# Kernel optimization log

Measured on AMD Instinct MI355X. Metric: run time of the kernel, lower is better.

## Reference

```python
import jax, jax.numpy as jnp
import numpy as np

WEIGHT_DECAY = 1e-4


def setup_inputs() -> dict:
    key = jax.random.key(0)
    k1, k2, k3 = jax.random.split(key, 3)
    # Linear weights: [out_features, in_features]
    w1 = jax.random.normal(k1, (4096, 4096), dtype=jnp.float32)
    w2 = jax.random.normal(k2, (8192, 2048), dtype=jnp.float32)
    w3 = jax.random.normal(k3, (2048, 8192), dtype=jnp.float32)
    return {"w1": w1, "w2": w2, "w3": w3}


def _spectral_norm(w):
    # torch.svd(weight) -> s sorted descending; max(s) == top singular value.
    s = jnp.linalg.svd(w, compute_uv=False)
    return jnp.max(s)


def reference(w1, w2, w3):
    # sum of largest singular values over all Linear weights, scaled by weight_decay
    spectral_reg = _spectral_norm(w1) + _spectral_norm(w2) + _spectral_norm(w3)
    return WEIGHT_DECAY * spectral_reg
```

## Files before the change

kernel.cpp:

```cpp
#include <hip/hip_runtime.h>
#include <math.h>


#define K_STEPS 24
#define VCAP 8192
#define MELEMS 16777216

#define UOFF   0
#define V0OFF  (3 * VCAP)
#define WOFF   (6 * VCAP)
#define P8OFF  (9 * VCAP)
#define P8TOT  3670016
#define BASOFF (P8OFF + P8TOT)
#define AL8OFF (BASOFF + 3 * K_STEPS * VCAP)
#define B28OFF (AL8OFF + 3 * K_STEPS)
#define NS2OFF (B28OFF + 3 * (K_STEPS + 1))
#define RQ2OFF (NS2OFF + 3)
#define VEC8_FLOATS (RQ2OFF + 3)

#define FB_AOFF (12 * VCAP)

typedef unsigned int u32;
typedef unsigned short u16;
typedef float f32x2 __attribute__((ext_vector_type(2)));

__device__ __forceinline__ int matN(int m) { return m == 0 ? 4096 : (m == 1 ? 2048 : 8192); }
__device__ __forceinline__ int pbase(int m) { return m == 0 ? 0 : (m == 1 ? 1048576 : 1572864); }

__device__ __forceinline__ f32x2 up8(u32 w, bool hi) {
    return hi ? __builtin_amdgcn_cvt_pk_f32_fp8(w, true)
              : __builtin_amdgcn_cvt_pk_f32_fp8(w, false);
}

__device__ float blockReduce(float v) {
    __shared__ float sh[16];
    int lane = threadIdx.x & 63, wid = threadIdx.x >> 6;
#pragma unroll
    for (int off = 32; off; off >>= 1) v += __shfl_down(v, off, 64);
    if (lane == 0) sh[wid] = v;
    __syncthreads();
    if (wid == 0) {
        int nw = (blockDim.x + 63) >> 6;
        float x = (lane < nw) ? sh[lane] : 0.0f;
#pragma unroll
        for (int off = 8; off; off >>= 1) x += __shfl_down(x, off, 64);
        if (lane == 0) sh[0] = x;
    }
    __syncthreads();
    float r = sh[0];
    __syncthreads();
    return r;
}


__global__ __launch_bounds__(1024) void k_init8(float* vec) {
    int bid = blockIdx.x, tid = threadIdx.x;
    if (bid < 3) {
        int mat = bid, n = matN(mat);
        float acc = 0.0f;
        for (int i = tid; i < VCAP; i += 1024) {
            float val = 0.0f;
            if (i < n) {
                unsigned h = (unsigned)(i * 2654435761u) ^ (0x9E3779B9u * (unsigned)(mat + 1));
                h ^= h >> 16; h *= 0x85EBCA6Bu; h ^= h >> 13; h *= 0xC2B2AE35u; h ^= h >> 16;
                val = ((h >> 8) * (1.0f / 16777216.0f)) - 0.5f;
                acc += val * val;
            }
            vec[UOFF + mat * VCAP + i] = val;
            vec[V0OFF + mat * VCAP + i] = 0.0f;
        }
        float nrm2 = blockReduce(acc);
        if (tid == 0) vec[B28OFF + mat * (K_STEPS + 1)] = nrm2;
    } else {
        for (int i = tid; i < 3 * K_STEPS; i += 1024) vec[AL8OFF + i] = 0.0f;
        for (int i = tid; i < 3 * (K_STEPS + 1); i += 1024)
            if (i % (K_STEPS + 1)) vec[B28OFF + i] = 0.0f;
        if (tid < 3) { vec[NS2OFF + tid] = 0.0f; vec[RQ2OFF + tid] = 0.0f; }
    }
}

__global__ __launch_bounds__(256) void k_convert8(const float* __restrict__ A0,
                                                  const float* __restrict__ A1,
                                                  const float* __restrict__ A2,
                                                  u32* __restrict__ F) {
    const int per_mat = MELEMS >> 3;
    const int nvec = 3 * per_mat;
    for (int i = blockIdx.x * 256 + threadIdx.x; i < nvec; i += gridDim.x * 256) {
        int mat = i >> 21;
        int iv = i & (per_mat - 1);
        const float4* Af = (const float4*)(mat == 0 ? A0 : (mat == 1 ? A1 : A2));
        float4 a = Af[2 * iv], b = Af[2 * iv + 1];
        u32 lo = __builtin_amdgcn_cvt_pk_fp8_f32(a.x, a.y, 0u, false);
        lo = __builtin_amdgcn_cvt_pk_fp8_f32(a.z, a.w, lo, true);
        u32 hi = __builtin_amdgcn_cvt_pk_fp8_f32(b.x, b.y, 0u, false);
        hi = __builtin_amdgcn_cvt_pk_fp8_f32(b.z, b.w, hi, true);
        uint2 o; o.x = lo; o.y = hi;
        ((uint2*)F)[i] = o;
    }
}

template <int N, int R>
__device__ void fusedAT_body(const u32* __restrict__ Fm, float* __restrict__ vec,
                             int mat, int chunk, int j,
                             float* __restrict__ Pm, float* wsh, float* shA) {
    constexpr int RPW = R / 4;
    constexpr int NU4 = N >> 4;
    constexpr int KK  = N >> 11;
    const int tid = threadIdx.x, wv = tid >> 6, lane = tid & 63;
    const int row0 = chunk * R;

    float inv = rsqrtf(vec[B28OFF + mat * (K_STEPS + 1) + j]);
    const float4* vp = (const float4*)(vec + UOFF + mat * VCAP);
    float aacc = 0.0f;
#pragma unroll
    for (int rr = 0; rr < RPW; ++rr) {
        int rl = wv * RPW + rr;
        const uint4* rp = (const uint4*)((const char*)Fm + (size_t)(row0 + rl) * N);
        float s = 0.0f;
#pragma unroll
        for (int c = lane; c < NU4; c += 64) {
            uint4 a = rp[c];
            float4 u0 = vp[4 * c + 0], u1 = vp[4 * c + 1];
            float4 u2 = vp[4 * c + 2], u3 = vp[4 * c + 3];
            f32x2 f0 = up8(a.x, false), f1 = up8(a.x, true);
            f32x2 f2 = up8(a.y, false), f3 = up8(a.y, true);
            f32x2 f4 = up8(a.z, false), f5 = up8(a.z, true);
            f32x2 f6 = up8(a.w, false), f7 = up8(a.w, true);
            s += f0[0] * u0.x + f0[1] * u0.y + f1[0] * u0.z + f1[1] * u0.w
               + f2[0] * u1.x + f2[1] * u1.y + f3[0] * u1.z + f3[1] * u1.w
               + f4[0] * u2.x + f4[1] * u2.y + f5[0] * u2.z + f5[1] * u2.w
               + f6[0] * u3.x + f6[1] * u3.y + f7[0] * u3.z + f7[1] * u3.w;
        }
#pragma unroll
        for (int off = 32; off; off >>= 1) s += __shfl_down(s, off, 64);
        if (lane == 0) { wsh[rl] = s * inv; aacc += s * s; }
    }
    if (lane == 0) shA[wv] = aacc;
    __syncthreads();
    if (tid == 0)
        atomicAdd(&vec[AL8OFF + mat * K_STEPS + j],
                  (shA[0] + shA[1] + shA[2] + shA[3]) * inv * inv);

#pragma unroll
    for (int kk = 0; kk < KK; ++kk) {
        int col = (tid + (kk << 8)) << 3;
        const char* bb = (const char*)Fm + (size_t)row0 * N + col;
        float a0 = 0, a1 = 0, a2 = 0, a3 = 0, a4 = 0, a5 = 0, a6 = 0, a7 = 0;
#pragma unroll 8
        for (int r = 0; r < R; ++r) {
            uint2 a = *(const uint2*)(bb + (size_t)r * N);
            f32x2 f0 = up8(a.x, false), f1 = up8(a.x, true);
            f32x2 f2 = up8(a.y, false), f3 = up8(a.y, true);
            float w = wsh[r];
            a0 += f0[0] * w; a1 += f0[1] * w; a2 += f1[0] * w; a3 += f1[1] * w;
            a4 += f2[0] * w; a5 += f2[1] * w; a6 += f3[0] * w; a7 += f3[1] * w;
        }
        float* Pp = Pm + (size_t)chunk * N + col;
        float4 lo = {a0, a1, a2, a3}, hi = {a4, a5, a6, a7};
        ((float4*)Pp)[0] = lo;
        ((float4*)Pp)[1] = hi;
    }
}

__global__ __launch_bounds__(256) void k_fusedAT(const u32* __restrict__ F,
                                                 float* __restrict__ vec, int j) {
    __shared__ float wsh[32];
    __shared__ float shA[4];
    int bid = blockIdx.x;
    if (bid < 256) {
        fusedAT_body<4096, 16>((const u32*)((const char*)F + (size_t)0 * MELEMS),
                               vec, 0, bid, j, vec + P8OFF + pbase(0), wsh, shA);
    } else if (bid < 512) {
        fusedAT_body<2048, 32>((const u32*)((const char*)F + (size_t)1 * MELEMS),
                               vec, 1, bid - 256, j, vec + P8OFF + pbase(1), wsh, shA);
    } else {
        fusedAT_body<8192, 8>((const u32*)((const char*)F + (size_t)2 * MELEMS),
                              vec, 2, bid - 512, j, vec + P8OFF + pbase(2), wsh, shA);
    }
}

__global__ __launch_bounds__(256) void k_stepR8(float* __restrict__ vec, int j) {
    int bid = blockIdx.x, tid = threadIdx.x;
    int mat, col0, n;
    if (bid < 16)      { mat = 0; n = 4096; col0 = bid << 8; }
    else if (bid < 24) { mat = 1; n = 2048; col0 = (bid - 16) << 8; }
    else               { mat = 2; n = 8192; col0 = (bid - 24) << 8; }
    int col = col0 + tid;
    const float* P = vec + P8OFF + pbase(mat);
    float z = 0.0f;
#pragma unroll 8
    for (int rc = 0; rc < 256; ++rc) z += P[(size_t)rc * n + col];
    float b2p = vec[B28OFF + mat * (K_STEPS + 1) + j];
    float bp = sqrtf(b2p);
    float inv = 1.0f / bp;
    float alpha = vec[AL8OFF + mat * K_STEPS + j];
    int g = mat * VCAP + col;
    float v1 = vec[UOFF + g] * inv;
    float r = z - alpha * v1 - bp * vec[V0OFF + g];
    vec[V0OFF + g] = v1;
    vec[UOFF + g] = r;
    vec[BASOFF + (mat * K_STEPS + j) * VCAP + col] = v1;
    float rr2 = blockReduce(r * r);
    if (tid == 0) atomicAdd(&vec[B28OFF + mat * (K_STEPS + 1) + j + 1], rr2);
}

__global__ __launch_bounds__(256) void k_final3(float* __restrict__ vec) {
    int bid = blockIdx.x;
    int mat = bid >> 2, q = bid & 3, tid = threadIdx.x, lane = tid & 63, wv = tid >> 6;
    int n = matN(mat);
    __shared__ double sa[K_STEPS], sb[K_STEPS];
    __shared__ double lamS;
    __shared__ float yl[K_STEPS];
    if (tid < K_STEPS) {
        sa[tid] = (double)vec[AL8OFF + mat * K_STEPS + tid];
        sb[tid] = (tid < K_STEPS - 1)
            ? sqrt((double)vec[B28OFF + mat * (K_STEPS + 1) + tid + 1]) : 0.0;
    }
    __syncthreads();
    if (wv == 0) {
        double g = 0.0;
        if (lane < K_STEPS) {
            double bl = lane ? sb[lane - 1] : 0.0;
            g = sa[lane] + bl + sb[lane];
        }
#pragma unroll
        for (int off = 32; off; off >>= 1) {
            double o = __shfl_xor(g, off, 64);
            if (o > g) g = o;
        }
        double lo = 0.0, hi = g > 0.0 ? g : 1.0;
        for (int round = 0; round < 4; ++round) {
            double step = (hi - lo) / 65.0;
            double x = lo + step * (double)(lane + 1);
            int cnt = 0;
            double d = 1.0;
            for (int i = 0; i < K_STEPS; ++i) {
                double off2 = 0.0;
                if (i) { double b = sb[i - 1]; off2 = b * b / d; }
                d = (sa[i] - x) - off2;
                if (d == 0.0) d = -1e-300;
                if (d < 0.0) cnt++;
            }
            unsigned long long mask = __ballot(cnt >= K_STEPS);
            if (mask) {
                int idx = __ffsll(mask) - 1;
                hi = lo + step * (double)(idx + 1);
                lo = lo + step * (double)idx;
            } else {
                lo = lo + step * 64.0;
            }
        }
        if (lane == 0) lamS = 0.5 * (lo + hi);
    }
    __syncthreads();
    if (tid == 0) {
        double lam2 = lamS * (1.0 + 1e-7);
        double x[K_STEPS], cp[K_STEPS];
        for (int i = 0; i < K_STEPS; ++i) x[i] = 1.0;
        for (int it = 0; it < 3; ++it) {
            double d = sa[0] - lam2;
            if (fabs(d) < 1e-14) d = (d < 0.0 ? -1e-14 : 1e-14);
            cp[0] = sb[0] / d;
            x[0] = x[0] / d;
            for (int i = 1; i < K_STEPS; ++i) {
                double m = (sa[i] - lam2) - sb[i - 1] * cp[i - 1];
                if (fabs(m) < 1e-14) m = (m < 0.0 ? -1e-14 : 1e-14);
                if (i < K_STEPS - 1) cp[i] = sb[i] / m;
                x[i] = (x[i] - sb[i - 1] * x[i - 1]) / m;
            }
            for (int i = K_STEPS - 2; i >= 0; --i) x[i] -= cp[i] * x[i + 1];
            double nr = 0.0;
            for (int i = 0; i < K_STEPS; ++i) nr += x[i] * x[i];
            nr = 1.0 / sqrt(nr);
            for (int i = 0; i < K_STEPS; ++i) x[i] *= nr;
        }
        for (int i = 0; i < K_STEPS; ++i) yl[i] = (float)x[i];
    }
    __syncthreads();
    int qn = n >> 2;
    int c0 = q * qn, c1 = c0 + qn;
    const float* BAS = vec + BASOFF + mat * K_STEPS * VCAP;
    float ns = 0.0f;
    for (int c = c0 + tid; c < c1; c += 256) {
        float acc = 0.0f;
#pragma unroll
        for (int jj = 0; jj < K_STEPS; ++jj) acc += yl[jj] * BAS[jj * VCAP + c];
        vec[WOFF + mat * VCAP + c] = acc;
        ns += acc * acc;
    }
    float t = blockReduce(ns);
    if (tid == 0) atomicAdd(&vec[NS2OFF + mat], t);
}

__global__ __launch_bounds__(1024) void k_rq(const float* __restrict__ A0,
                                             const float* __restrict__ A1,
                                             const float* __restrict__ A2,
                                             float* __restrict__ vec) {
    __shared__ float shA[16];
    int bid = blockIdx.x, tid = threadIdx.x, wv = tid >> 6, lane = tid & 63;
    int mat, row0, n;
    if (bid < 256)      { mat = 0; n = 4096; row0 = bid << 4; }
    else if (bid < 768) { mat = 1; n = 2048; row0 = (bid - 256) << 4; }
    else                { mat = 2; n = 8192; row0 = (bid - 768) << 4; }
    const float* A = mat == 0 ? A0 : (mat == 1 ? A1 : A2);
    int row = row0 + wv;
    const float4* rp = (const float4*)(A + (size_t)row * n);
    const float4* vp = (const float4*)(vec + WOFF + mat * VCAP);
    int nf4 = n >> 2;
    float s = 0.0f;
    for (int c = lane; c < nf4; c += 64) {
        float4 a = rp[c], v = vp[c];
        s += a.x * v.x + a.y * v.y + a.z * v.z + a.w * v.w;
    }
#pragma unroll
    for (int off = 32; off; off >>= 1) s += __shfl_down(s, off, 64);
    if (lane == 0) shA[wv] = s * s;
    __syncthreads();
    if (tid == 0) {
        float t = 0.0f;
#pragma unroll
        for (int k = 0; k < 16; ++k) t += shA[k];
        atomicAdd(&vec[RQ2OFF + mat], t);
    }
}

__global__ void k_out(const float* __restrict__ vec, float* __restrict__ out) {
    if (threadIdx.x == 0 && blockIdx.x == 0) {
        float s = 0.0f;
        for (int m = 0; m < 3; ++m)
            s += sqrtf(vec[RQ2OFF + m] / vec[NS2OFF + m]);
        out[0] = 1e-4f * s;
    }
}

__global__ __launch_bounds__(1024) void k_init(float* vec) {
    int mat = blockIdx.x;
    int n = matN(mat);
    float* V0 = vec + mat * VCAP;
    float* V1 = vec + 3 * VCAP + mat * VCAP;
    float* Z  = vec + 9 * VCAP + mat * VCAP;
    int tid = threadIdx.x;
    float acc = 0.0f;
    for (int i = tid; i < VCAP; i += 1024) {
        float val = 0.0f;
        if (i < n) {
            unsigned h = (unsigned)(i * 2654435761u) ^ (0x9E3779B9u * (unsigned)(mat + 1));
            h ^= h >> 16; h *= 0x85EBCA6Bu; h ^= h >> 13; h *= 0xC2B2AE35u; h ^= h >> 16;
            val = ((h >> 8) * (1.0f / 16777216.0f)) - 0.5f;
            acc += val * val;
        }
        V1[i] = val; V0[i] = 0.0f; Z[i] = 0.0f;
    }
    float nrm2 = blockReduce(acc);
    float inv = rsqrtf(nrm2);
    for (int i = tid; i < n; i += 1024) V1[i] *= inv;
}

__global__ __launch_bounds__(256) void k_gemvA(const float* __restrict__ A0,
                                               const float* __restrict__ A1,
                                               const float* __restrict__ A2,
                                               float* __restrict__ vec) {
    const float* V1 = vec + 3 * VCAP;
    float* W = vec + 6 * VCAP;
    int wid = (int)((blockIdx.x * blockDim.x + threadIdx.x) >> 6);
    int lane = threadIdx.x & 63;
    int mat, row;
    if (wid < 4096)       { mat = 0; row = wid; }
    else if (wid < 12288) { mat = 1; row = wid - 4096; }
    else                  { mat = 2; row = wid - 12288; }
    const float* A = mat == 0 ? A0 : (mat == 1 ? A1 : A2);
    int n = matN(mat);
    const float4* rowp = (const float4*)(A + (size_t)row * n);
    const float4* vp = (const float4*)(V1 + mat * VCAP);
    int nf4 = n >> 2;
    float s = 0.0f;
    for (int t = lane; t < nf4; t += 64) {
        float4 a = rowp[t], v = vp[t];
        s += a.x * v.x + a.y * v.y + a.z * v.z + a.w * v.w;
    }
#pragma unroll
    for (int off = 32; off; off >>= 1) s += __shfl_down(s, off, 64);
    if (lane == 0) W[mat * VCAP + row] = s;
}

__global__ __launch_bounds__(256) void k_gemvT(const float* __restrict__ A0,
                                               const float* __restrict__ A1,
                                               const float* __restrict__ A2,
                                               float* __restrict__ vec) {
    const float* W = vec + 6 * VCAP;
    float* Z = vec + 9 * VCAP;
    int bid = blockIdx.x;
    int mat = bid >> 8;
    int t = bid & 255;
    int n = matN(mat);
    int nColTiles = n >> 10;
    int colTile = t % nColTiles;
    int rowChunk = t / nColTiles;
    int r0 = rowChunk * 64;
    int col = colTile * 1024 + threadIdx.x * 4;
    const float* A = mat == 0 ? A0 : (mat == 1 ? A1 : A2);
    __shared__ float wsh[64];
    if (threadIdx.x < 64) wsh[threadIdx.x] = W[mat * VCAP + r0 + threadIdx.x];
    __syncthreads();
    const float* Ab = A + (size_t)r0 * n + col;
    float4 s = {0.0f, 0.0f, 0.0f, 0.0f};
#pragma unroll 4
    for (int r = 0; r < 64; ++r) {
        float4 a = *(const float4*)(Ab + (size_t)r * n);
        float w = wsh[r];
        s.x += a.x * w; s.y += a.y * w; s.z += a.z * w; s.w += a.w * w;
    }
    float* Zm = Z + mat * VCAP + col;
    atomicAdd(Zm + 0, s.x);
    atomicAdd(Zm + 1, s.y);
    atomicAdd(Zm + 2, s.z);
    atomicAdd(Zm + 3, s.w);
}

__global__ __launch_bounds__(1024) void k_update(float* __restrict__ vec, int j) {
    int mat = blockIdx.x;
    int n = matN(mat);
    float* V0 = vec + mat * VCAP;
    float* V1 = vec + 3 * VCAP + mat * VCAP;
    float* Z  = vec + 9 * VCAP + mat * VCAP;
    float* ALPHA = vec + FB_AOFF;
    float* BETA  = ALPHA + 3 * K_STEPS;
    int tid = threadIdx.x;
    float acc = 0.0f;
    for (int i = tid; i < n; i += 1024) acc += V1[i] * Z[i];
    float alpha = blockReduce(acc);
    float bp = (j > 0) ? BETA[mat * K_STEPS + j - 1] : 0.0f;
    float acc2 = 0.0f;
    for (int i = tid; i < n; i += 1024) {
        float v1 = V1[i];
        float r = Z[i] - alpha * v1 - bp * V0[i];
        V0[i] = v1;
        Z[i] = r;
        acc2 += r * r;
    }
    float b2 = blockReduce(acc2);
    float beta = sqrtf(b2);
    float inv = (beta > 1e-20f) ? (1.0f / beta) : 0.0f;
    for (int i = tid; i < n; i += 1024) {
        V1[i] = Z[i] * inv;
        Z[i] = 0.0f;
    }
    if (tid == 0) {
        ALPHA[mat * K_STEPS + j] = alpha;
        BETA[mat * K_STEPS + j] = beta;
    }
}

__global__ __launch_bounds__(256) void k_final2(const float* __restrict__ vec,
                                                float* __restrict__ out) {
    __shared__ double sa[3][K_STEPS], sb[3][K_STEPS];
    __shared__ double sig[3];
    int tid = threadIdx.x, wid = tid >> 6, lane = tid & 63;
    if (wid < 3 && lane < K_STEPS) {
        const float* AL = vec + FB_AOFF + wid * K_STEPS;
        const float* BE = vec + FB_AOFF + 3 * K_STEPS + wid * K_STEPS;
        sa[wid][lane] = (double)AL[lane];
        sb[wid][lane] = (lane < K_STEPS - 1) ? (double)BE[lane] : 0.0;
    }
    __syncthreads();
    if (wid < 3) {
        double g = 0.0;
        if (lane < K_STEPS) {
            double bl_ = lane ? sb[wid][lane - 1] : 0.0;
            g = sa[wid][lane] + bl_ + sb[wid][lane];
        }
#pragma unroll
        for (int off = 32; off; off >>= 1) {
            double o = __shfl_xor(g, off, 64);
            if (o > g) g = o;
        }
        double lo = 0.0, hi = g > 0.0 ? g : 1.0;
        for (int round = 0; round < 4; ++round) {
            double step = (hi - lo) / 65.0;
            double x = lo + step * (double)(lane + 1);
            int cnt = 0;
            double d = 1.0;
            for (int i = 0; i < K_STEPS; ++i) {
                double off2 = 0.0;
                if (i) { double b = sb[wid][i - 1]; off2 = b * b / d; }
                d = (sa[wid][i] - x) - off2;
                if (d == 0.0) d = -1e-300;
                if (d < 0.0) cnt++;
            }
            unsigned long long mask = __ballot(cnt >= K_STEPS);
            if (mask) {
                int idx = __ffsll(mask) - 1;
                hi = lo + step * (double)(idx + 1);
                lo = lo + step * (double)idx;
            } else {
                lo = lo + step * 64.0;
            }
        }
        if (lane == 0) {
            double lam = 0.5 * (lo + hi);
            sig[wid] = sqrt(lam > 0.0 ? lam : 0.0);
        }
    }
    __syncthreads();
    if (tid == 0) out[0] = (float)(1e-4 * (sig[0] + sig[1] + sig[2]));
}

extern "C" void kernel_launch(void* const* d_in, const int* in_sizes, int n_in,
                              void* d_out, int out_size, void* d_ws, size_t ws_size,
                              hipStream_t stream) {
    const float* A0 = (const float*)d_in[0];
    const float* A1 = (const float*)d_in[1];
    const float* A2 = (const float*)d_in[2];
    float* out = (float*)d_out;

    const size_t f8_bytes = (size_t)3 * MELEMS;
    const size_t vec8_bytes = (size_t)VEC8_FLOATS * 4 + 1024;

    if (ws_size >= f8_bytes + vec8_bytes) {
        u32* F = (u32*)d_ws;
        float* vec = (float*)((char*)d_ws + f8_bytes);
        hipLaunchKernelGGL(k_init8, dim3(4), dim3(1024), 0, stream, vec);
        hipLaunchKernelGGL(k_convert8, dim3(3072), dim3(256), 0, stream, A0, A1, A2, F);
        for (int j = 0; j < K_STEPS; ++j) {
            hipLaunchKernelGGL(k_fusedAT, dim3(768), dim3(256), 0, stream, F, vec, j);
            hipLaunchKernelGGL(k_stepR8, dim3(56), dim3(256), 0, stream, vec, j);
        }
        hipLaunchKernelGGL(k_final3, dim3(12), dim3(256), 0, stream, vec);
        hipLaunchKernelGGL(k_rq, dim3(896), dim3(1024), 0, stream, A0, A1, A2, vec);
        hipLaunchKernelGGL(k_out, dim3(1), dim3(64), 0, stream, vec, out);
    } else {
        float* vec = (float*)d_ws;
        hipLaunchKernelGGL(k_init, dim3(3), dim3(1024), 0, stream, vec);
        for (int j = 0; j < K_STEPS; ++j) {
            hipLaunchKernelGGL(k_gemvA, dim3(3584), dim3(256), 0, stream, A0, A1, A2, vec);
            hipLaunchKernelGGL(k_gemvT, dim3(768), dim3(256), 0, stream, A0, A1, A2, vec);
            hipLaunchKernelGGL(k_update, dim3(3), dim3(1024), 0, stream, vec, j);
        }
        hipLaunchKernelGGL(k_final2, dim3(1), dim3(256), 0, stream, vec, out);
    }
}
```

Measured before the change: 898.2 us.

## Stage FP8 row tile in shared memory, halve rows per block, fuse convert/init

```diff
diff --git a/kernel.cpp b/kernel.cpp
--- a/kernel.cpp
+++ b/kernel.cpp
@@ -10,7 +10,7 @@
 #define V0OFF  (3 * VCAP)
 #define WOFF   (6 * VCAP)
 #define P8OFF  (9 * VCAP)
-#define P8TOT  3670016
+#define P8TOT  7340032
 #define BASOFF (P8OFF + P8TOT)
 #define AL8OFF (BASOFF + 3 * K_STEPS * VCAP)
 #define B28OFF (AL8OFF + 3 * K_STEPS)
@@ -25,7 +25,7 @@
 typedef float f32x2 __attribute__((ext_vector_type(2)));
 
 __device__ __forceinline__ int matN(int m) { return m == 0 ? 4096 : (m == 1 ? 2048 : 8192); }
-__device__ __forceinline__ int pbase(int m) { return m == 0 ? 0 : (m == 1 ? 1048576 : 1572864); }
+__device__ __forceinline__ int pbase(int m) { return m == 0 ? 0 : (m == 1 ? 2097152 : 3145728); }
 
 __device__ __forceinline__ f32x2 up8(u32 w, bool hi) {
     return hi ? __builtin_amdgcn_cvt_pk_f32_fp8(w, true)
@@ -53,12 +53,36 @@
 }
 
 
-__global__ __launch_bounds__(1024) void k_init8(float* vec) {
+__global__ __launch_bounds__(256) void k_conv_init(const float* __restrict__ A0,
+                                                   const float* __restrict__ A1,
+                                                   const float* __restrict__ A2,
+                                                   u32* __restrict__ F,
+                                                   float* __restrict__ vec) {
     int bid = blockIdx.x, tid = threadIdx.x;
-    if (bid < 3) {
-        int mat = bid, n = matN(mat);
+    if (bid < 3072) {
+        const int per16 = MELEMS >> 4;
+        const int nvec16 = 3 * per16;
+        for (int i = bid * 256 + tid; i < nvec16; i += 3072 * 256) {
+            int mat = i >> 20;
+            int iv = i & (per16 - 1);
+            const float4* Af = (const float4*)(mat == 0 ? A0 : (mat == 1 ? A1 : A2));
+            float4 a = Af[4 * iv + 0], b = Af[4 * iv + 1];
+            float4 c = Af[4 * iv + 2], d = Af[4 * iv + 3];
+            uint4 o;
+            o.x = __builtin_amdgcn_cvt_pk_fp8_f32(a.x, a.y, 0u, false);
+            o.x = __builtin_amdgcn_cvt_pk_fp8_f32(a.z, a.w, o.x, true);
+            o.y = __builtin_amdgcn_cvt_pk_fp8_f32(b.x, b.y, 0u, false);
+            o.y = __builtin_amdgcn_cvt_pk_fp8_f32(b.z, b.w, o.y, true);
+            o.z = __builtin_amdgcn_cvt_pk_fp8_f32(c.x, c.y, 0u, false);
+            o.z = __builtin_amdgcn_cvt_pk_fp8_f32(c.z, c.w, o.z, true);
+            o.w = __builtin_amdgcn_cvt_pk_fp8_f32(d.x, d.y, 0u, false);
+            o.w = __builtin_amdgcn_cvt_pk_fp8_f32(d.z, d.w, o.w, true);
+            ((uint4*)F)[i] = o;
+        }
+    } else if (bid < 3075) {
+        int mat = bid - 3072, n = matN(mat);
         float acc = 0.0f;
-        for (int i = tid; i < VCAP; i += 1024) {
+        for (int i = tid; i < VCAP; i += 256) {
             float val = 0.0f;
             if (i < n) {
                 unsigned h = (unsigned)(i * 2654435761u) ^ (0x9E3779B9u * (unsigned)(mat + 1));
@@ -72,39 +96,21 @@
         float nrm2 = blockReduce(acc);
         if (tid == 0) vec[B28OFF + mat * (K_STEPS + 1)] = nrm2;
     } else {
-        for (int i = tid; i < 3 * K_STEPS; i += 1024) vec[AL8OFF + i] = 0.0f;
-        for (int i = tid; i < 3 * (K_STEPS + 1); i += 1024)
+        for (int i = tid; i < 3 * K_STEPS; i += 256) vec[AL8OFF + i] = 0.0f;
+        for (int i = tid; i < 3 * (K_STEPS + 1); i += 256)
             if (i % (K_STEPS + 1)) vec[B28OFF + i] = 0.0f;
         if (tid < 3) { vec[NS2OFF + tid] = 0.0f; vec[RQ2OFF + tid] = 0.0f; }
-    }
-}
-
-__global__ __launch_bounds__(256) void k_convert8(const float* __restrict__ A0,
-                                                  const float* __restrict__ A1,
-                                                  const float* __restrict__ A2,
-                                                  u32* __restrict__ F) {
-    const int per_mat = MELEMS >> 3;
-    const int nvec = 3 * per_mat;
-    for (int i = blockIdx.x * 256 + threadIdx.x; i < nvec; i += gridDim.x * 256) {
-        int mat = i >> 21;
-        int iv = i & (per_mat - 1);
-        const float4* Af = (const float4*)(mat == 0 ? A0 : (mat == 1 ? A1 : A2));
-        float4 a = Af[2 * iv], b = Af[2 * iv + 1];
-        u32 lo = __builtin_amdgcn_cvt_pk_fp8_f32(a.x, a.y, 0u, false);
-        lo = __builtin_amdgcn_cvt_pk_fp8_f32(a.z, a.w, lo, true);
-        u32 hi = __builtin_amdgcn_cvt_pk_fp8_f32(b.x, b.y, 0u, false);
-        hi = __builtin_amdgcn_cvt_pk_fp8_f32(b.z, b.w, hi, true);
-        uint2 o; o.x = lo; o.y = hi;
-        ((uint2*)F)[i] = o;
     }
 }
 
 template <int N, int R>
 __device__ void fusedAT_body(const u32* __restrict__ Fm, float* __restrict__ vec,
                              int mat, int chunk, int j,
-                             float* __restrict__ Pm, float* wsh, float* shA) {
+                             float* __restrict__ Pm, uint4* tile4,
+                             float* wsh, float* shA) {
     constexpr int RPW = R / 4;
     constexpr int NU4 = N >> 4;
+    constexpr int NU2 = N >> 3;
     constexpr int KK  = N >> 11;
     const int tid = threadIdx.x, wv = tid >> 6, lane = tid & 63;
     const int row0 = chunk * R;
@@ -120,6 +126,7 @@
 #pragma unroll
         for (int c = lane; c < NU4; c += 64) {
             uint4 a = rp[c];
+            tile4[rl * NU4 + c] = a;
             float4 u0 = vp[4 * c + 0], u1 = vp[4 * c + 1];
             float4 u2 = vp[4 * c + 2], u3 = vp[4 * c + 3];
             f32x2 f0 = up8(a.x, false), f1 = up8(a.x, true);
@@ -141,21 +148,21 @@
         atomicAdd(&vec[AL8OFF + mat * K_STEPS + j],
                   (shA[0] + shA[1] + shA[2] + shA[3]) * inv * inv);
 
+    const uint2* t2 = (const uint2*)tile4;
 #pragma unroll
     for (int kk = 0; kk < KK; ++kk) {
-        int col = (tid + (kk << 8)) << 3;
-        const char* bb = (const char*)Fm + (size_t)row0 * N + col;
+        int cidx = tid + (kk << 8);
         float a0 = 0, a1 = 0, a2 = 0, a3 = 0, a4 = 0, a5 = 0, a6 = 0, a7 = 0;
-#pragma unroll 8
+#pragma unroll
         for (int r = 0; r < R; ++r) {
-            uint2 a = *(const uint2*)(bb + (size_t)r * N);
+            uint2 a = t2[r * NU2 + cidx];
             f32x2 f0 = up8(a.x, false), f1 = up8(a.x, true);
             f32x2 f2 = up8(a.y, false), f3 = up8(a.y, true);
             float w = wsh[r];
             a0 += f0[0] * w; a1 += f0[1] * w; a2 += f1[0] * w; a3 += f1[1] * w;
             a4 += f2[0] * w; a5 += f2[1] * w; a6 += f3[0] * w; a7 += f3[1] * w;
         }
-        float* Pp = Pm + (size_t)chunk * N + col;
+        float* Pp = Pm + (size_t)chunk * N + (cidx << 3);
         float4 lo = {a0, a1, a2, a3}, hi = {a4, a5, a6, a7};
         ((float4*)Pp)[0] = lo;
         ((float4*)Pp)[1] = hi;
@@ -164,18 +171,19 @@
 
 __global__ __launch_bounds__(256) void k_fusedAT(const u32* __restrict__ F,
                                                  float* __restrict__ vec, int j) {
-    __shared__ float wsh[32];
+    __shared__ uint4 tile4[2048];
+    __shared__ float wsh[16];
     __shared__ float shA[4];
     int bid = blockIdx.x;
-    if (bid < 256) {
-        fusedAT_body<4096, 16>((const u32*)((const char*)F + (size_t)0 * MELEMS),
-                               vec, 0, bid, j, vec + P8OFF + pbase(0), wsh, shA);
-    } else if (bid < 512) {
-        fusedAT_body<2048, 32>((const u32*)((const char*)F + (size_t)1 * MELEMS),
-                               vec, 1, bid - 256, j, vec + P8OFF + pbase(1), wsh, shA);
+    if (bid < 512) {
+        fusedAT_body<4096, 8>((const u32*)((const char*)F + (size_t)0 * MELEMS),
+                              vec, 0, bid, j, vec + P8OFF + pbase(0), tile4, wsh, shA);
+    } else if (bid < 1024) {
+        fusedAT_body<2048, 16>((const u32*)((const char*)F + (size_t)1 * MELEMS),
+                               vec, 1, bid - 512, j, vec + P8OFF + pbase(1), tile4, wsh, shA);
     } else {
-        fusedAT_body<8192, 8>((const u32*)((const char*)F + (size_t)2 * MELEMS),
-                              vec, 2, bid - 512, j, vec + P8OFF + pbase(2), wsh, shA);
+        fusedAT_body<8192, 4>((const u32*)((const char*)F + (size_t)2 * MELEMS),
+                              vec, 2, bid - 1024, j, vec + P8OFF + pbase(2), tile4, wsh, shA);
     }
 }
 
@@ -189,7 +197,7 @@
     const float* P = vec + P8OFF + pbase(mat);
     float z = 0.0f;
 #pragma unroll 8
-    for (int rc = 0; rc < 256; ++rc) z += P[(size_t)rc * n + col];
+    for (int rc = 0; rc < 512; ++rc) z += P[(size_t)rc * n + col];
     float b2p = vec[B28OFF + mat * (K_STEPS + 1) + j];
     float bp = sqrtf(b2p);
     float inv = 1.0f / bp;
@@ -519,10 +527,9 @@
     if (ws_size >= f8_bytes + vec8_bytes) {
         u32* F = (u32*)d_ws;
         float* vec = (float*)((char*)d_ws + f8_bytes);
-        hipLaunchKernelGGL(k_init8, dim3(4), dim3(1024), 0, stream, vec);
-        hipLaunchKernelGGL(k_convert8, dim3(3072), dim3(256), 0, stream, A0, A1, A2, F);
+        hipLaunchKernelGGL(k_conv_init, dim3(3076), dim3(256), 0, stream, A0, A1, A2, F, vec);
         for (int j = 0; j < K_STEPS; ++j) {
-            hipLaunchKernelGGL(k_fusedAT, dim3(768), dim3(256), 0, stream, F, vec, j);
+            hipLaunchKernelGGL(k_fusedAT, dim3(1536), dim3(256), 0, stream, F, vec, j);
             hipLaunchKernelGGL(k_stepR8, dim3(56), dim3(256), 0, stream, vec, j);
         }
         hipLaunchKernelGGL(k_final3, dim3(12), dim3(256), 0, stream, vec);
```

Result: slower. 1.293 ms (+43.9%).

## Fuse fp32-to-fp8 conversion into first Lanczos matvec iteration

Applied to the files above, without the earlier changes.

```diff
diff --git a/kernel.cpp b/kernel.cpp
--- a/kernel.cpp
+++ b/kernel.cpp
@@ -5,6 +5,7 @@
 #define K_STEPS 24
 #define VCAP 8192
 #define MELEMS 16777216
+#define NCHUNK 256
 
 #define UOFF   0
 #define V0OFF  (3 * VCAP)
@@ -21,7 +22,6 @@
 #define FB_AOFF (12 * VCAP)
 
 typedef unsigned int u32;
-typedef unsigned short u16;
 typedef float f32x2 __attribute__((ext_vector_type(2)));
 
 __device__ __forceinline__ int matN(int m) { return m == 0 ? 4096 : (m == 1 ? 2048 : 8192); }
@@ -53,12 +53,12 @@
 }
 
 
-__global__ __launch_bounds__(1024) void k_init8(float* vec) {
+__global__ __launch_bounds__(256) void k_init8(float* vec) {
     int bid = blockIdx.x, tid = threadIdx.x;
     if (bid < 3) {
         int mat = bid, n = matN(mat);
         float acc = 0.0f;
-        for (int i = tid; i < VCAP; i += 1024) {
+        for (int i = tid; i < VCAP; i += 256) {
             float val = 0.0f;
             if (i < n) {
                 unsigned h = (unsigned)(i * 2654435761u) ^ (0x9E3779B9u * (unsigned)(mat + 1));
@@ -72,30 +72,106 @@
         float nrm2 = blockReduce(acc);
         if (tid == 0) vec[B28OFF + mat * (K_STEPS + 1)] = nrm2;
     } else {
-        for (int i = tid; i < 3 * K_STEPS; i += 1024) vec[AL8OFF + i] = 0.0f;
-        for (int i = tid; i < 3 * (K_STEPS + 1); i += 1024)
+        for (int i = tid; i < 3 * K_STEPS; i += 256) vec[AL8OFF + i] = 0.0f;
+        for (int i = tid; i < 3 * (K_STEPS + 1); i += 256)
             if (i % (K_STEPS + 1)) vec[B28OFF + i] = 0.0f;
         if (tid < 3) { vec[NS2OFF + tid] = 0.0f; vec[RQ2OFF + tid] = 0.0f; }
     }
 }
 
-__global__ __launch_bounds__(256) void k_convert8(const float* __restrict__ A0,
+template <int N, int R>
+__device__ void fusedAT0_body(const float* __restrict__ Am, u32* __restrict__ Fm,
+                              float* __restrict__ vec, int mat, int chunk,
+                              float* __restrict__ Pm, float* wsh, float* shA) {
+    constexpr int RPW = R / 4;
+    constexpr int NU4 = N >> 4;
+    constexpr int KK  = N >> 11;
+    const int tid = threadIdx.x, wv = tid >> 6, lane = tid & 63;
+    const int row0 = chunk * R;
+
+    float inv = rsqrtf(vec[B28OFF + mat * (K_STEPS + 1)]);
+    const float4* vp = (const float4*)(vec + UOFF + mat * VCAP);
+    float aacc = 0.0f;
+#pragma unroll
+    for (int rr = 0; rr < RPW; ++rr) {
+        int rl = wv * RPW + rr;
+        int row = row0 + rl;
+        const float4* Ar = (const float4*)(Am + (size_t)row * N);
+        uint4* Fr = (uint4*)((char*)Fm + (size_t)row * N);
+        float s = 0.0f;
+#pragma unroll
+        for (int c = lane; c < NU4; c += 64) {
+            float4 a0 = Ar[4 * c + 0], a1 = Ar[4 * c + 1];
+            float4 a2 = Ar[4 * c + 2], a3 = Ar[4 * c + 3];
+            uint4 o;
+            o.x = __builtin_amdgcn_cvt_pk_fp8_f32(a0.x, a0.y, 0u, false);
+            o.x = __builtin_amdgcn_cvt_pk_fp8_f32(a0.z, a0.w, o.x, true);
+            o.y = __builtin_amdgcn_cvt_pk_fp8_f32(a1.x, a1.y, 0u, false);
+            o.y = __builtin_amdgcn_cvt_pk_fp8_f32(a1.z, a1.w, o.y, true);
+            o.z = __builtin_amdgcn_cvt_pk_fp8_f32(a2.x, a2.y, 0u, false);
+            o.z = __builtin_amdgcn_cvt_pk_fp8_f32(a2.z, a2.w, o.z, true);
+            o.w = __builtin_amdgcn_cvt_pk_fp8_f32(a3.x, a3.y, 0u, false);
+            o.w = __builtin_amdgcn_cvt_pk_fp8_f32(a3.z, a3.w, o.w, true);
+            Fr[c] = o;
+            float4 u0 = vp[4 * c + 0], u1 = vp[4 * c + 1];
+            float4 u2 = vp[4 * c + 2], u3 = vp[4 * c + 3];
+            f32x2 f0 = up8(o.x, false), f1 = up8(o.x, true);
+            f32x2 f2 = up8(o.y, false), f3 = up8(o.y, true);
+            f32x2 f4 = up8(o.z, false), f5 = up8(o.z, true);
+            f32x2 f6 = up8(o.w, false), f7 = up8(o.w, true);
+            s += f0[0] * u0.x + f0[1] * u0.y + f1[0] * u0.z + f1[1] * u0.w
+               + f2[0] * u1.x + f2[1] * u1.y + f3[0] * u1.z + f3[1] * u1.w
+               + f4[0] * u2.x + f4[1] * u2.y + f5[0] * u2.z + f5[1] * u2.w
+               + f6[0] * u3.x + f6[1] * u3.y + f7[0] * u3.z + f7[1] * u3.w;
+        }
+#pragma unroll
+        for (int off = 32; off; off >>= 1) s += __shfl_down(s, off, 64);
+        if (lane == 0) { wsh[rl] = s * inv; aacc += s * s; }
+    }
+    if (lane == 0) shA[wv] = aacc;
+    __syncthreads();
+    if (tid == 0)
+        atomicAdd(&vec[AL8OFF + mat * K_STEPS],
+                  (shA[0] + shA[1] + shA[2] + shA[3]) * inv * inv);
+
+#pragma unroll
+    for (int kk = 0; kk < KK; ++kk) {
+        int col = (tid + (kk << 8)) << 3;
+        const char* bb = (const char*)Fm + (size_t)row0 * N + col;
+        float a0 = 0, a1 = 0, a2 = 0, a3 = 0, a4 = 0, a5 = 0, a6 = 0, a7 = 0;
+#pragma unroll 8
+        for (int r = 0; r < R; ++r) {
+            uint2 a = *(const uint2*)(bb + (size_t)r * N);
+            f32x2 f0 = up8(a.x, false), f1 = up8(a.x, true);
+            f32x2 f2 = up8(a.y, false), f3 = up8(a.y, true);
+            float w = wsh[r];
+            a0 += f0[0] * w; a1 += f0[1] * w; a2 += f1[0] * w; a3 += f1[1] * w;
+            a4 += f2[0] * w; a5 += f2[1] * w; a6 += f3[0] * w; a7 += f3[1] * w;
+        }
+        float* Pp = Pm + (size_t)chunk * N + col;
+        float4 lo = {a0, a1, a2, a3}, hi = {a4, a5, a6, a7};
+        ((float4*)Pp)[0] = lo;
+        ((float4*)Pp)[1] = hi;
+    }
+}
+
+__global__ __launch_bounds__(256) void k_fusedAT0(const float* __restrict__ A0,
                                                   const float* __restrict__ A1,
                                                   const float* __restrict__ A2,
-                                                  u32* __restrict__ F) {
-    const int per_mat = MELEMS >> 3;
-    const int nvec = 3 * per_mat;
-    for (int i = blockIdx.x * 256 + threadIdx.x; i < nvec; i += gridDim.x * 256) {
-        int mat = i >> 21;
-        int iv = i & (per_mat - 1);
-        const float4* Af = (const float4*)(mat == 0 ? A0 : (mat == 1 ? A1 : A2));
-        float4 a = Af[2 * iv], b = Af[2 * iv + 1];
-        u32 lo = __builtin_amdgcn_cvt_pk_fp8_f32(a.x, a.y, 0u, false);
-        lo = __builtin_amdgcn_cvt_pk_fp8_f32(a.z, a.w, lo, true);
-        u32 hi = __builtin_amdgcn_cvt_pk_fp8_f32(b.x, b.y, 0u, false);
-        hi = __builtin_amdgcn_cvt_pk_fp8_f32(b.z, b.w, hi, true);
-        uint2 o; o.x = lo; o.y = hi;
-        ((uint2*)F)[i] = o;
+                                                  u32* __restrict__ F,
+                                                  float* __restrict__ vec) {
+    __shared__ float wsh[32];
+    __shared__ float shA[4];
+    int bid = blockIdx.x;
+    if (bid < 256) {
+        fusedAT0_body<4096, 16>(A0, (u32*)((char*)F + (size_t)0 * MELEMS),
+                                vec, 0, bid, vec + P8OFF + pbase(0), wsh, shA);
+    } else if (bid < 512) {
+        fusedAT0_body<2048, 32>(A1, (u32*)((char*)F + (size_t)1 * MELEMS),
+                                vec, 1, bid - 256, vec + P8OFF + pbase(1), wsh, shA);
+    } else {
+        fusedAT0_body<8192, 8>(A2, (u32*)((char*)F + (size_t)2 * MELEMS),
+                               vec, 2, bid - 512, vec + P8OFF + pbase(2), wsh, shA);
     }
 }
 
@@ -189,7 +265,7 @@
     const float* P = vec + P8OFF + pbase(mat);
     float z = 0.0f;
 #pragma unroll 8
-    for (int rc = 0; rc < 256; ++rc) z += P[(size_t)rc * n + col];
+    for (int rc = 0; rc < NCHUNK; ++rc) z += P[(size_t)rc * n + col];
     float b2p = vec[B28OFF + mat * (K_STEPS + 1) + j];
     float bp = sqrtf(b2p);
     float inv = 1.0f / bp;
@@ -519,9 +595,10 @@
     if (ws_size >= f8_bytes + vec8_bytes) {
         u32* F = (u32*)d_ws;
         float* vec = (float*)((char*)d_ws + f8_bytes);
-        hipLaunchKernelGGL(k_init8, dim3(4), dim3(1024), 0, stream, vec);
-        hipLaunchKernelGGL(k_convert8, dim3(3072), dim3(256), 0, stream, A0, A1, A2, F);
-        for (int j = 0; j < K_STEPS; ++j) {
+        hipLaunchKernelGGL(k_init8, dim3(4), dim3(256), 0, stream, vec);
+        hipLaunchKernelGGL(k_fusedAT0, dim3(768), dim3(256), 0, stream, A0, A1, A2, F, vec);
+        hipLaunchKernelGGL(k_stepR8, dim3(56), dim3(256), 0, stream, vec, 0);
+        for (int j = 1; j < K_STEPS; ++j) {
             hipLaunchKernelGGL(k_fusedAT, dim3(768), dim3(256), 0, stream, F, vec, j);
             hipLaunchKernelGGL(k_stepR8, dim3(56), dim3(256), 0, stream, vec, j);
         }
```

After: 892.4 us. Within noise of the previous version (-0.6%).
